# Performance work log

Measured on AMD Instinct MI355X. Metric: run time of the kernel, lower is better.

## Reference

```python
import jax, jax.numpy as jnp
import numpy as np

B, N, DIM, H, DH = 2, 2048, 512, 8, 64
INNER = H * DH  # == DIM, required by the q.view trick in the original module
STEP = 4


def setup_inputs() -> dict:
    key = jax.random.key(0)
    k1, k2, k3 = jax.random.split(key, 3)
    x = jax.random.normal(k1, (B, N, DIM), jnp.float32)
    # to_qkv: Linear(dim, 4*inner_dim, bias=False); stored as [in, out] for x @ W
    W_qkv = jax.random.normal(k2, (DIM, 4 * INNER), jnp.float32) * 0.02
    # to_out: Linear(2*inner_dim, dim) with bias
    W_out = jax.random.normal(k3, (2 * INNER, DIM), jnp.float32) * 0.02
    b_out = jnp.zeros((DIM,), jnp.float32)
    return {"x": x, "W_qkv": W_qkv, "W_out": W_out, "b_out": b_out}


def reference(x, W_qkv, W_out, b_out):
    b, n, _ = x.shape
    h, dh = H, DH
    scale = dh ** -0.5

    qkvt = x @ W_qkv                       # [b, n, 4*inner]
    q, k, v, t = jnp.split(qkvt, 4, axis=-1)
    to_heads = lambda z: z.reshape(b, n, h, dh).transpose(0, 2, 1, 3)  # [b,h,n,dh]
    q, k, v, t = map(to_heads, (q, k, v, t))

    # pad q by repeating its last row yushu times (note: yushu=4 when n%4==0)
    yushu = STEP - n % STEP
    q = jnp.concatenate([q, jnp.repeat(q[:, :, -1:, :], yushu, axis=2)], axis=2)
    q0 = q.reshape(b, h, STEP, (n + yushu) // STEP, dh)[:, :, 0]  # [b,h,(n+yushu)/4,dh]
    q = jnp.tile(q0, (1, 1, STEP, 1))[:, :, :n]                   # [b,h,n,dh]

    dots = jnp.einsum('bhnd,bhmd->bhnm', q, k) * scale
    attn1 = jax.nn.softmax(dots, axis=-1)

    # fixed distance-decay attention: exp(-|i-j|/e), column-normalized
    pos = jnp.arange(1, n + 1, dtype=x.dtype)
    tg = jnp.abs(pos[None, :] - pos[:, None])                     # [n, n]
    attn2 = jnp.exp(-tg / jnp.exp(jnp.asarray(1.0, x.dtype)))
    # torch: attn2 / attn2.sum(-1) broadcasts [n] over last axis (divides column j by row-sum j)
    attn2 = attn2 / attn2.sum(-1)

    out1 = jnp.einsum('bhnm,bhmd->bhnd', attn1, v)
    out2 = jnp.einsum('nm,bhmd->bhnd', attn2, t)  # attn2 shared across b,h; no repeat needed
    out = jnp.concatenate([out1, out2], axis=-1)   # [b,h,n,2*dh]
    out = out.transpose(0, 2, 1, 3).reshape(b, n, 2 * h * dh)  # b n (h d)
    return out @ W_out + b_out  # dropout=0.0 -> identity
```

## Files before the change

### kernel.cpp

```cpp
#include <hip/hip_runtime.h>

#define NSEQ 2048
#define NB   2
#define NH   8

typedef unsigned short u16;
typedef __attribute__((ext_vector_type(8))) short s8v;
typedef __attribute__((ext_vector_type(4))) float f4v;

static __device__ __forceinline__ u16 f2bf(float f) {
  unsigned u = __float_as_uint(f);
  unsigned r = (u + 0x7fffu + ((u >> 16) & 1u)) >> 16;
  return (u16)r;
}
static __device__ __forceinline__ unsigned pk2(float a, float b) {
  return (unsigned)f2bf(a) | ((unsigned)f2bf(b) << 16);
}
static __device__ __forceinline__ float bf2f(u16 v) {
  return __uint_as_float(((unsigned)v) << 16);
}

typedef __attribute__((address_space(3))) unsigned int lds_u32;
typedef const __attribute__((address_space(1))) unsigned int glob_u32;
static __device__ __forceinline__ void load16(const void* g, void* l) {
  __builtin_amdgcn_global_load_lds((glob_u32*)g, (lds_u32*)l, 16, 0, 0);
}

__global__ __launch_bounds__(256)
void prep_kernel(const float* __restrict__ x, const float* __restrict__ Wqkv,
                 const float* __restrict__ Wout, u16* __restrict__ xb,
                 u16* __restrict__ WqkvT, u16* __restrict__ Wc) {
  __shared__ float tile[32][33];
  const int bid = blockIdx.x;
  if (bid < 1024) {
    long i = ((long)bid * 256 + threadIdx.x) * 8;
    float4 a = *(const float4*)&x[i];
    float4 b = *(const float4*)&x[i + 4];
    uint4 w;
    w.x = pk2(a.x, a.y); w.y = pk2(a.z, a.w);
    w.z = pk2(b.x, b.y); w.w = pk2(b.z, b.w);
    *(uint4*)&xb[i] = w;
    return;
  }
  const int tx = threadIdx.x & 31, ty = threadIdx.x >> 5;
  if (bid < 2048) {
    int b2 = bid - 1024;
    int c0 = (b2 & 63) * 32, r0 = (b2 >> 6) * 32;
#pragma unroll
    for (int s = 0; s < 32; s += 8)
      tile[ty + s][tx] = Wqkv[(long)(r0 + ty + s) * 2048 + c0 + tx];
    __syncthreads();
#pragma unroll
    for (int s = 0; s < 32; s += 8)
      WqkvT[(long)(c0 + ty + s) * 512 + r0 + tx] = f2bf(tile[tx][ty + s]);
    return;
  }
  {
    int b3 = bid - 2048;
    int part = b3 >= 256;
    if (part) b3 -= 256;
    int c0 = (b3 & 15) * 32, r0 = (b3 >> 4) * 32;
#pragma unroll
    for (int s = 0; s < 32; s += 8) {
      int k = r0 + ty + s;
      int srcrow = ((k >> 6) * 128) + part * 64 + (k & 63);
      tile[ty + s][tx] = Wout[(long)srcrow * 512 + c0 + tx];
    }
    __syncthreads();
    int koff = part ? 0 : 512;
#pragma unroll
    for (int s = 0; s < 32; s += 8) {
      long o = (long)(c0 + ty + s) * 1024 + koff + r0 + tx;
      Wc[o] = f2bf(tile[tx][ty + s]);
    }
  }
}

__global__ __launch_bounds__(256)
void gemm1_fused(const u16* __restrict__ xb, const u16* __restrict__ WqkvT,
                 u16* __restrict__ qkvtb, u16* __restrict__ qu,
                 u16* __restrict__ VtG) {
  const int bx = blockIdx.x, by = blockIdx.y;
  const bool isq = bx >= 12;
  if (isq && by >= 9) return;
  __shared__ alignas(16) u16 As[128 * 32];
  __shared__ alignas(16) u16 Bs[128 * 32];
  const int tid = threadIdx.x, lane = tid & 63, wave = tid >> 6;
  const int l15 = lane & 15, quad = lane >> 4;
  const int wr = wave >> 1, wc = wave & 1;
  const int Brow0 = isq ? (bx - 12) * 128 : 512 + bx * 128;

  f4v acc[4][4];
#pragma unroll
  for (int i = 0; i < 4; ++i)
#pragma unroll
    for (int j = 0; j < 4; ++j) acc[i][j] = (f4v){0.f, 0.f, 0.f, 0.f};

  for (int k0 = 0; k0 < 512; k0 += 32) {
    __syncthreads();
#pragma unroll
    for (int c = 0; c < 2; ++c) {
      int off = (c * 4 + wave) * 1024 + lane * 16;
      int r = off >> 6, cb = (off & 63) >> 1;
      int gar;
      if (!isq) {
        gar = by * 128 + r;
      } else {
        int rr = by * 128 + r;
        int b = rr >= 576;
        int s = rr - (b ? 576 : 0);
        if (s >= 513) s -= 513;
        gar = b * 2048 + s;
      }
      load16(&xb[(long)gar * 512 + k0 + cb], ((char*)As) + off);
      load16(&WqkvT[(long)(Brow0 + r) * 512 + k0 + cb], ((char*)Bs) + off);
    }
    __syncthreads();

    s8v bf[4];
#pragma unroll
    for (int j = 0; j < 4; ++j)
      bf[j] = *(const s8v*)&Bs[(wc * 64 + j * 16 + l15) * 32 + quad * 8];
#pragma unroll
    for (int i = 0; i < 4; ++i) {
      s8v af = *(const s8v*)&As[(wr * 64 + i * 16 + l15) * 32 + quad * 8];
#pragma unroll
      for (int j = 0; j < 4; ++j)
        acc[i][j] = __builtin_amdgcn_mfma_f32_16x16x32_bf16(af, bf[j], acc[i][j], 0, 0, 0);
    }
  }

  const bool isv = (!isq) && bx >= 4 && bx < 8;
#pragma unroll
  for (int i = 0; i < 4; ++i) {
    int row0 = by * 128 + wr * 64 + i * 16 + quad * 4;
    if (isv) {
      int b = row0 >> 11, n = row0 & 2047;
#pragma unroll
      for (int j = 0; j < 4; ++j) {
        int vcol = (bx - 4) * 128 + wc * 64 + j * 16 + l15;
        int h = vcol >> 6, d = vcol & 63;
        uint2 w;
        w.x = pk2(acc[i][j][0], acc[i][j][1]);
        w.y = pk2(acc[i][j][2], acc[i][j][3]);
        *(uint2*)&VtG[(((long)b * 8 + h) * 64 + d) * 2048 + n] = w;
      }
    } else {
#pragma unroll
      for (int rr = 0; rr < 4; ++rr) {
        int row = row0 + rr;
#pragma unroll
        for (int j = 0; j < 4; ++j) {
          int col = wc * 64 + j * 16 + l15;
          u16 v = f2bf(acc[i][j][rr]);
          if (!isq)
            qkvtb[(long)row * 2048 + 512 + bx * 128 + col] = v;
          else
            qu[(long)row * 512 + (bx - 12) * 128 + col] = v;
        }
      }
    }
  }
}

__global__ __launch_bounds__(256)
void gemm2_merged(const u16* __restrict__ O2, const u16* __restrict__ O1u,
                  const u16* __restrict__ Wc, const float* __restrict__ bias,
                  float* __restrict__ C) {
  __shared__ alignas(16) u16 As[128 * 32];
  __shared__ alignas(16) u16 Bs[64 * 32];
  const int tid = threadIdx.x, lane = tid & 63, wave = tid >> 6;
  const int l15 = lane & 15, quad = lane >> 4;
  const int wr = wave >> 1, wc = wave & 1;
  const long m0 = (long)blockIdx.y * 128, n0 = (long)blockIdx.x * 64;

  long baseO2[2], baseO1[2];
  int offA[2];
#pragma unroll
  for (int c = 0; c < 2; ++c) {
    int off = (c * 4 + wave) * 1024 + lane * 16;
    int r = off >> 6, cb = (off & 63) >> 1;
    offA[c] = off;
    long rowA = m0 + r;
    int b = (int)(rowA >> 11);
    int eff = (int)(rowA & 2047) % 513;
    baseO2[c] = rowA * 512 + cb;
    baseO1[c] = ((long)(b * 576 + eff)) * 512 + cb;
  }
  const int offB = wave * 1024 + lane * 16;
  const long baseB = (long)(n0 + (offB >> 6)) * 1024 + ((offB & 63) >> 1);

  f4v acc[4][2];
#pragma unroll
  for (int i = 0; i < 4; ++i)
#pragma unroll
    for (int j = 0; j < 2; ++j) acc[i][j] = (f4v){0.f, 0.f, 0.f, 0.f};

  for (int k0 = 0; k0 < 1024; k0 += 32) {
    __syncthreads();
#pragma unroll
    for (int c = 0; c < 2; ++c) {
      const u16* src = (k0 < 512) ? &O2[baseO2[c] + k0] : &O1u[baseO1[c] + k0 - 512];
      load16(src, ((char*)As) + offA[c]);
    }
    load16(&Wc[baseB + k0], ((char*)Bs) + offB);
    __syncthreads();

    s8v bf[2];
#pragma unroll
    for (int j = 0; j < 2; ++j)
      bf[j] = *(const s8v*)&Bs[(wc * 32 + j * 16 + l15) * 32 + quad * 8];
#pragma unroll
    for (int i = 0; i < 4; ++i) {
      s8v af = *(const s8v*)&As[(wr * 64 + i * 16 + l15) * 32 + quad * 8];
#pragma unroll
      for (int j = 0; j < 2; ++j)
        acc[i][j] = __builtin_amdgcn_mfma_f32_16x16x32_bf16(af, bf[j], acc[i][j], 0, 0, 0);
    }
  }

#pragma unroll
  for (int i = 0; i < 4; ++i)
#pragma unroll
    for (int rr = 0; rr < 4; ++rr) {
      long row = m0 + wr * 64 + i * 16 + quad * 4 + rr;
#pragma unroll
      for (int j = 0; j < 2; ++j) {
        long col = n0 + wc * 32 + j * 16 + l15;
        C[row * 512 + col] = acc[i][j][rr] + bias[col];
      }
    }
}

__global__ __launch_bounds__(256)
void attn_kernel(const u16* __restrict__ qkvt, const u16* __restrict__ qu,
                 const u16* __restrict__ VtG, float* __restrict__ Opart,
                 float* __restrict__ rspart) {
  __shared__ alignas(16) u16 Qs[64 * 64];
  __shared__ alignas(16) u16 Ks[64 * 64];
  __shared__ alignas(16) u16 Vt[64 * 64];
  __shared__ alignas(16) u16 Ps[4][16][72];

  const int tid  = threadIdx.x;
  const int lane = tid & 63, wave = tid >> 6;
  const int l15  = lane & 15, quad = lane >> 4;
  const int qtile = blockIdx.x;
  const int bh = blockIdx.y;
  const int split = blockIdx.z;
  const int b = bh >> 3, h = bh & 7;
  const long rowbase = (long)b * NSEQ;
  const long vtbase = ((long)b * 8 + h) * 64 * 2048;

  int srow[2], scs[2];
#pragma unroll
  for (int p = 0; p < 2; ++p) {
    int idx = p * 256 + tid;
    srow[p] = idx >> 3;
    scs[p] = (idx & 7) ^ (srow[p] & 7);
  }

#pragma unroll
  for (int p = 0; p < 2; ++p) {
    int v = qtile * 64 + srow[p];
    int eff = v >= 513 ? v - 513 : v;
    load16(&qu[((long)(b * 576 + eff)) * 512 + h * 64 + scs[p] * 8],
           (char*)Qs + (p * 256 + wave * 64) * 16);
  }
  __syncthreads();

  s8v qf[2];
  {
    const int mrow = wave * 16 + l15;
    const int c0 = quad ^ (mrow & 7);
    qf[0] = *(const s8v*)&Qs[mrow * 64 + c0 * 8];
    qf[1] = *(const s8v*)&Qs[mrow * 64 + (c0 ^ 4) * 8];
  }

  f4v oacc[4];
#pragma unroll
  for (int i = 0; i < 4; ++i) oacc[i] = (f4v){0.f, 0.f, 0.f, 0.f};
  float rs[4] = {0.f, 0.f, 0.f, 0.f};

  for (int kt = 0; kt < 8; ++kt) {
    __syncthreads();
    const int kb = split * 512 + kt * 64;
#pragma unroll
    for (int p = 0; p < 2; ++p) {
      load16(&qkvt[(rowbase + kb + srow[p]) * 2048 + 512 + h * 64 + scs[p] * 8],
             (char*)Ks + (p * 256 + wave * 64) * 16);
      load16(&VtG[vtbase + (long)srow[p] * 2048 + kb + scs[p] * 8],
             (char*)Vt + (p * 256 + wave * 64) * 16);
    }
    __syncthreads();

#pragma unroll
    for (int nt = 0; nt < 4; ++nt) {
      f4v s = {0.f, 0.f, 0.f, 0.f};
      const int kr = nt * 16 + l15;
      const int kc0 = quad ^ (kr & 7);
      s8v kf0 = *(const s8v*)&Ks[kr * 64 + kc0 * 8];
      s8v kf1 = *(const s8v*)&Ks[kr * 64 + (kc0 ^ 4) * 8];
      s = __builtin_amdgcn_mfma_f32_16x16x32_bf16(qf[0], kf0, s, 0, 0, 0);
      s = __builtin_amdgcn_mfma_f32_16x16x32_bf16(qf[1], kf1, s, 0, 0, 0);
#pragma unroll
      for (int rr = 0; rr < 4; ++rr) {
        float p = __expf(s[rr] * 0.125f);
        rs[rr] += p;
        Ps[wave][quad * 4 + rr][nt * 16 + l15] = f2bf(p);
      }
    }
    asm volatile("" ::: "memory");

    s8v pf0 = *(const s8v*)&Ps[wave][l15][quad * 8];
    s8v pf1 = *(const s8v*)&Ps[wave][l15][32 + quad * 8];
#pragma unroll
    for (int nt = 0; nt < 4; ++nt) {
      const int vr = nt * 16 + l15;
      const int vc0 = quad ^ (vr & 7);
      s8v vf0 = *(const s8v*)&Vt[vr * 64 + vc0 * 8];
      s8v vf1 = *(const s8v*)&Vt[vr * 64 + (vc0 ^ 4) * 8];
      oacc[nt] = __builtin_amdgcn_mfma_f32_16x16x32_bf16(pf0, vf0, oacc[nt], 0, 0, 0);
      oacc[nt] = __builtin_amdgcn_mfma_f32_16x16x32_bf16(pf1, vf1, oacc[nt], 0, 0, 0);
    }
  }

  const long sb = ((long)split * 16 + bh) * 576;
#pragma unroll
  for (int rr = 0; rr < 4; ++rr) {
    float t = rs[rr];
    t += __shfl_xor(t, 1);
    t += __shfl_xor(t, 2);
    t += __shfl_xor(t, 4);
    t += __shfl_xor(t, 8);
    int row = qtile * 64 + wave * 16 + quad * 4 + rr;
    if (l15 == 0) rspart[sb + row] = t;
#pragma unroll
    for (int nt = 0; nt < 4; ++nt)
      Opart[(sb + row) * 64 + nt * 16 + l15] = oacc[nt][rr];
  }
}

__global__ __launch_bounds__(256)
void post_kernel(const u16* __restrict__ qkvt, const float* __restrict__ Opart,
                 const float* __restrict__ rspart, u16* __restrict__ O1u,
                 u16* __restrict__ O2) {
  __shared__ u16 Ts[256 * 64];
  __shared__ float Is[256];
  const int tid = threadIdx.x;
  const int bid = blockIdx.x;
  if (bid >= 512) {
    int idx = (bid - 512) * 256 + tid;
    int d4 = idx & 15, rowbh = idx >> 4;
    int bh = rowbh / 576, row = rowbh - bh * 576;
    int b = bh >> 3, h = bh & 7;
    float4 o = {0.f, 0.f, 0.f, 0.f};
    float rsum = 0.f;
#pragma unroll
    for (int s = 0; s < 4; ++s) {
      long base = ((long)s * 16 + bh) * 576 + row;
      float4 v = *(const float4*)&Opart[base * 64 + d4 * 4];
      o.x += v.x; o.y += v.y; o.z += v.z; o.w += v.w;
      rsum += rspart[base];
    }
    float inv = 1.0f / rsum;
    uint2 w = {pk2(o.x * inv, o.y * inv), pk2(o.z * inv, o.w * inv)};
    *(uint2*)&O1u[((long)(b * 576 + row)) * 512 + h * 64 + d4 * 4] = w;
    return;
  }
  const int rg = bid & 31;
  const int bh = bid >> 5;
  const int b = bh >> 3, h = bh & 7;
  const int g0 = rg * 64 - 96;
#pragma unroll
  for (int c = 0; c < 8; ++c) {
    int chunk = c * 256 + tid;
    int row = chunk >> 3, cc = chunk & 7;
    int gr = g0 + row;
    uint4 w = {0u, 0u, 0u, 0u};
    if (gr >= 0 && gr < NSEQ)
      w = *(const uint4*)&qkvt[((long)(b * NSEQ + gr)) * 2048 + 1536 + h * 64 + cc * 8];
    *(uint4*)&Ts[row * 64 + cc * 8] = w;
  }
  {
    const float ie = 0.36787944117144233f;
    const float rr = 0.69220062755534635f;
    const float inv1mr = 1.0f / (1.0f - rr);
    int gr = g0 + tid;
    float val = 0.f;
    if (gr >= 0 && gr < NSEQ) {
      float rj = __expf(-ie * (float)gr);
      float rn = __expf(-ie * (float)(NSEQ - 1 - gr));
      float s = 1.0f + (rr - rr * rj) * inv1mr + (rr - rr * rn) * inv1mr;
      val = 1.0f / s;
    }
    Is[tid] = val;
  }
  __syncthreads();

  const int d = tid & 63, sub = tid >> 6;
  const float r = 0.69220062755534635f;
  const int lo = 96 + sub * 16;
  float F = 0.f;
  float Fv[16];
#pragma unroll 8
  for (int j = lo - 96; j < lo; ++j)
    F = F * r + Is[j] * bf2f(Ts[j * 64 + d]);
#pragma unroll
  for (int k = 0; k < 16; ++k) {
    int j = lo + k;
    F = F * r + Is[j] * bf2f(Ts[j * 64 + d]);
    Fv[k] = F;
  }
  float G = 0.f;
#pragma unroll 8
  for (int j = lo + 15 + 96; j > lo + 15; --j)
    G = G * r + Is[j] * bf2f(Ts[j * 64 + d]);
#pragma unroll
  for (int k = 15; k >= 0; --k) {
    int j = lo + k;
    float u = Is[j] * bf2f(Ts[j * 64 + d]);
    G = G * r + u;
    O2[((long)(b * NSEQ + g0 + j)) * 512 + h * 64 + d] = f2bf(Fv[k] + G - u);
  }
}

extern "C" void kernel_launch(void* const* d_in, const int* in_sizes, int n_in,
                              void* d_out, int out_size, void* d_ws, size_t ws_size,
                              hipStream_t stream) {
  (void)in_sizes; (void)n_in; (void)out_size; (void)ws_size;
  const float* x    = (const float*)d_in[0];
  const float* Wqkv = (const float*)d_in[1];
  const float* Wout = (const float*)d_in[2];
  const float* bout = (const float*)d_in[3];
  float* out = (float*)d_out;

  u16*   qkvtb = (u16*)d_ws;
  u16*   qu    = qkvtb + (size_t)4096 * 2048;
  u16*   VtG   = qu    + (size_t)1152 * 512;
  u16*   O2    = VtG   + (size_t)2 * 8 * 64 * 2048;
  u16*   O1u   = O2    + (size_t)4096 * 512;
  u16*   xb    = O1u   + (size_t)1152 * 512;
  u16*   WqkvT = xb    + (size_t)4096 * 512;
  u16*   Wc    = WqkvT + (size_t)2048 * 512;
  float* Opart = (float*)(Wc + (size_t)512 * 1024);
  float* rsp   = Opart + (size_t)4 * 16 * 576 * 64;

  prep_kernel<<<dim3(2560), 256, 0, stream>>>(x, Wqkv, Wout, xb, WqkvT, Wc);
  gemm1_fused<<<dim3(16, 32), 256, 0, stream>>>(xb, WqkvT, qkvtb, qu, VtG);
  attn_kernel<<<dim3(9, 16, 4), 256, 0, stream>>>(qkvtb, qu, VtG, Opart, rsp);
  post_kernel<<<dim3(1088), 256, 0, stream>>>(qkvtb, Opart, rsp, O1u, O2);
  gemm2_merged<<<dim3(8, 32), 256, 0, stream>>>(O2, O1u, Wc, bout, out);
}
```

Baseline: 132.9 us.

## Double GEMM K-tile with swizzled LDS, co-schedule out2 with attention, bf16 partials

Both GEMM kernels now stage 64-wide K tiles in XOR-swizzled shared memory, which halves the number of barrier pairs and avoids bank conflicts. The distance-decay (out2) work moves out of the post kernel into the attention launch as extra blocks that share a union of shared memory, so it runs alongside the softmax attention blocks. The remaining combine step becomes its own small kernel. Attention partial outputs are stored as bf16 instead of fp32, which cuts partial-buffer traffic at some precision cost. The larger shared footprint may lower occupancy.

```diff
diff --git a/kernel.cpp b/kernel.cpp
--- a/kernel.cpp
+++ b/kernel.cpp
@@ -83,50 +83,65 @@
   const int bx = blockIdx.x, by = blockIdx.y;
   const bool isq = bx >= 12;
   if (isq && by >= 9) return;
-  __shared__ alignas(16) u16 As[128 * 32];
-  __shared__ alignas(16) u16 Bs[128 * 32];
+  __shared__ alignas(16) u16 As[128 * 64];
+  __shared__ alignas(16) u16 Bs[128 * 64];
   const int tid = threadIdx.x, lane = tid & 63, wave = tid >> 6;
   const int l15 = lane & 15, quad = lane >> 4;
   const int wr = wave >> 1, wc = wave & 1;
   const int Brow0 = isq ? (bx - 12) * 128 : 512 + bx * 128;
 
+  int offv[4];
+  long baseA[4], baseB[4];
+#pragma unroll
+  for (int c = 0; c < 4; ++c) {
+    int off = (c * 4 + wave) * 1024 + lane * 16;
+    int r = off >> 7;
+    int cp = (off & 127) >> 4;
+    int cb = ((cp ^ (r & 7)) << 3);
+    offv[c] = off;
+    int gar;
+    if (!isq) {
+      gar = by * 128 + r;
+    } else {
+      int rr = by * 128 + r;
+      int b = rr >= 576;
+      int s = rr - (b ? 576 : 0);
+      if (s >= 513) s -= 513;
+      gar = b * 2048 + s;
+    }
+    baseA[c] = (long)gar * 512 + cb;
+    baseB[c] = (long)(Brow0 + r) * 512 + cb;
+  }
+
   f4v acc[4][4];
 #pragma unroll
   for (int i = 0; i < 4; ++i)
 #pragma unroll
     for (int j = 0; j < 4; ++j) acc[i][j] = (f4v){0.f, 0.f, 0.f, 0.f};
 
-  for (int k0 = 0; k0 < 512; k0 += 32) {
-    __syncthreads();
-#pragma unroll
-    for (int c = 0; c < 2; ++c) {
-      int off = (c * 4 + wave) * 1024 + lane * 16;
-      int r = off >> 6, cb = (off & 63) >> 1;
-      int gar;
-      if (!isq) {
-        gar = by * 128 + r;
-      } else {
-        int rr = by * 128 + r;
-        int b = rr >= 576;
-        int s = rr - (b ? 576 : 0);
-        if (s >= 513) s -= 513;
-        gar = b * 2048 + s;
-      }
-      load16(&xb[(long)gar * 512 + k0 + cb], ((char*)As) + off);
-      load16(&WqkvT[(long)(Brow0 + r) * 512 + k0 + cb], ((char*)Bs) + off);
-    }
-    __syncthreads();
-
-    s8v bf[4];
-#pragma unroll
-    for (int j = 0; j < 4; ++j)
-      bf[j] = *(const s8v*)&Bs[(wc * 64 + j * 16 + l15) * 32 + quad * 8];
-#pragma unroll
-    for (int i = 0; i < 4; ++i) {
-      s8v af = *(const s8v*)&As[(wr * 64 + i * 16 + l15) * 32 + quad * 8];
+  for (int k0 = 0; k0 < 512; k0 += 64) {
+    __syncthreads();
+#pragma unroll
+    for (int c = 0; c < 4; ++c) {
+      load16(&xb[baseA[c] + k0], ((char*)As) + offv[c]);
+      load16(&WqkvT[baseB[c] + k0], ((char*)Bs) + offv[c]);
+    }
+    __syncthreads();
+
+#pragma unroll
+    for (int ksub = 0; ksub < 2; ++ksub) {
+      const int cc = (((ksub << 2) | quad) ^ (l15 & 7)) << 3;
+      s8v bf[4];
 #pragma unroll
       for (int j = 0; j < 4; ++j)
-        acc[i][j] = __builtin_amdgcn_mfma_f32_16x16x32_bf16(af, bf[j], acc[i][j], 0, 0, 0);
+        bf[j] = *(const s8v*)&Bs[(wc * 64 + j * 16 + l15) * 64 + cc];
+#pragma unroll
+      for (int i = 0; i < 4; ++i) {
+        s8v af = *(const s8v*)&As[(wr * 64 + i * 16 + l15) * 64 + cc];
+#pragma unroll
+        for (int j = 0; j < 4; ++j)
+          acc[i][j] = __builtin_amdgcn_mfma_f32_16x16x32_bf16(af, bf[j], acc[i][j], 0, 0, 0);
+      }
     }
   }
 
@@ -167,19 +182,20 @@
 void gemm2_merged(const u16* __restrict__ O2, const u16* __restrict__ O1u,
                   const u16* __restrict__ Wc, const float* __restrict__ bias,
                   float* __restrict__ C) {
-  __shared__ alignas(16) u16 As[128 * 32];
-  __shared__ alignas(16) u16 Bs[64 * 32];
+  __shared__ alignas(16) u16 As[128 * 64];
+  __shared__ alignas(16) u16 Bs[64 * 64];
   const int tid = threadIdx.x, lane = tid & 63, wave = tid >> 6;
   const int l15 = lane & 15, quad = lane >> 4;
   const int wr = wave >> 1, wc = wave & 1;
   const long m0 = (long)blockIdx.y * 128, n0 = (long)blockIdx.x * 64;
 
-  long baseO2[2], baseO1[2];
-  int offA[2];
-#pragma unroll
-  for (int c = 0; c < 2; ++c) {
+  int offA[4];
+  long baseO2[4], baseO1[4];
+#pragma unroll
+  for (int c = 0; c < 4; ++c) {
     int off = (c * 4 + wave) * 1024 + lane * 16;
-    int r = off >> 6, cb = (off & 63) >> 1;
+    int r = off >> 7, cp = (off & 127) >> 4;
+    int cb = ((cp ^ (r & 7)) << 3);
     offA[c] = off;
     long rowA = m0 + r;
     int b = (int)(rowA >> 11);
@@ -187,8 +203,16 @@
     baseO2[c] = rowA * 512 + cb;
     baseO1[c] = ((long)(b * 576 + eff)) * 512 + cb;
   }
-  const int offB = wave * 1024 + lane * 16;
-  const long baseB = (long)(n0 + (offB >> 6)) * 1024 + ((offB & 63) >> 1);
+  int offB[2];
+  long baseB[2];
+#pragma unroll
+  for (int c = 0; c < 2; ++c) {
+    int off = (c * 4 + wave) * 1024 + lane * 16;
+    int r = off >> 7, cp = (off & 127) >> 4;
+    int cb = ((cp ^ (r & 7)) << 3);
+    offB[c] = off;
+    baseB[c] = (long)(n0 + r) * 1024 + cb;
+  }
 
   f4v acc[4][2];
 #pragma unroll
@@ -196,26 +220,32 @@
 #pragma unroll
     for (int j = 0; j < 2; ++j) acc[i][j] = (f4v){0.f, 0.f, 0.f, 0.f};
 
-  for (int k0 = 0; k0 < 1024; k0 += 32) {
-    __syncthreads();
-#pragma unroll
-    for (int c = 0; c < 2; ++c) {
+  for (int k0 = 0; k0 < 1024; k0 += 64) {
+    __syncthreads();
+#pragma unroll
+    for (int c = 0; c < 4; ++c) {
       const u16* src = (k0 < 512) ? &O2[baseO2[c] + k0] : &O1u[baseO1[c] + k0 - 512];
       load16(src, ((char*)As) + offA[c]);
     }
-    load16(&Wc[baseB + k0], ((char*)Bs) + offB);
-    __syncthreads();
-
-    s8v bf[2];
-#pragma unroll
-    for (int j = 0; j < 2; ++j)
-      bf[j] = *(const s8v*)&Bs[(wc * 32 + j * 16 + l15) * 32 + quad * 8];
-#pragma unroll
-    for (int i = 0; i < 4; ++i) {
-      s8v af = *(const s8v*)&As[(wr * 64 + i * 16 + l15) * 32 + quad * 8];
+#pragma unroll
+    for (int c = 0; c < 2; ++c)
+      load16(&Wc[baseB[c] + k0], ((char*)Bs) + offB[c]);
+    __syncthreads();
+
+#pragma unroll
+    for (int ksub = 0; ksub < 2; ++ksub) {
+      const int cc = (((ksub << 2) | quad) ^ (l15 & 7)) << 3;
+      s8v bf[2];
 #pragma unroll
       for (int j = 0; j < 2; ++j)
-        acc[i][j] = __builtin_amdgcn_mfma_f32_16x16x32_bf16(af, bf[j], acc[i][j], 0, 0, 0);
+        bf[j] = *(const s8v*)&Bs[(wc * 32 + j * 16 + l15) * 64 + cc];
+#pragma unroll
+      for (int i = 0; i < 4; ++i) {
+        s8v af = *(const s8v*)&As[(wr * 64 + i * 16 + l15) * 64 + cc];
+#pragma unroll
+        for (int j = 0; j < 2; ++j)
+          acc[i][j] = __builtin_amdgcn_mfma_f32_16x16x32_bf16(af, bf[j], acc[i][j], 0, 0, 0);
+      }
     }
   }
 
@@ -232,21 +262,91 @@
     }
 }
 
+struct AttnSm {
+  alignas(16) u16 Qs[64 * 64];
+  alignas(16) u16 Ks[64 * 64];
+  alignas(16) u16 Vt[64 * 64];
+  alignas(16) u16 Ps[4][16][72];
+};
+struct Out2Sm {
+  alignas(16) u16 Ts[256 * 64];
+  float Is[256];
+};
+
 __global__ __launch_bounds__(256)
-void attn_kernel(const u16* __restrict__ qkvt, const u16* __restrict__ qu,
-                 const u16* __restrict__ VtG, float* __restrict__ Opart,
-                 float* __restrict__ rspart) {
-  __shared__ alignas(16) u16 Qs[64 * 64];
-  __shared__ alignas(16) u16 Ks[64 * 64];
-  __shared__ alignas(16) u16 Vt[64 * 64];
-  __shared__ alignas(16) u16 Ps[4][16][72];
-
-  const int tid  = threadIdx.x;
+void attn_out2(const u16* __restrict__ qkvt, const u16* __restrict__ qu,
+               const u16* __restrict__ VtG, u16* __restrict__ Opart,
+               float* __restrict__ rspart, u16* __restrict__ O2) {
+  __shared__ union { AttnSm a; Out2Sm o; } sm;
+  const int tid = threadIdx.x;
+  const int bid = blockIdx.x;
+
+  if (bid >= 576) {
+    const int bid2 = bid - 576;
+    const int rg = bid2 & 31;
+    const int bh = bid2 >> 5;
+    const int b = bh >> 3, h = bh & 7;
+    const int g0 = rg * 64 - 96;
+#pragma unroll
+    for (int c = 0; c < 8; ++c) {
+      int chunk = c * 256 + tid;
+      int row = chunk >> 3, cc = chunk & 7;
+      int gr = g0 + row;
+      uint4 w = {0u, 0u, 0u, 0u};
+      if (gr >= 0 && gr < NSEQ)
+        w = *(const uint4*)&qkvt[((long)(b * NSEQ + gr)) * 2048 + 1536 + h * 64 + cc * 8];
+      *(uint4*)&sm.o.Ts[row * 64 + cc * 8] = w;
+    }
+    {
+      const float ie = 0.36787944117144233f;
+      const float rr = 0.69220062755534635f;
+      const float inv1mr = 1.0f / (1.0f - rr);
+      int gr = g0 + tid;
+      float val = 0.f;
+      if (gr >= 0 && gr < NSEQ) {
+        float rj = __expf(-ie * (float)gr);
+        float rn = __expf(-ie * (float)(NSEQ - 1 - gr));
+        float s = 1.0f + (rr - rr * rj) * inv1mr + (rr - rr * rn) * inv1mr;
+        val = 1.0f / s;
+      }
+      sm.o.Is[tid] = val;
+    }
+    __syncthreads();
+
+    const int d = tid & 63, sub = tid >> 6;
+    const float r = 0.69220062755534635f;
+    const int lo = 96 + sub * 16;
+    float F = 0.f;
+    float Fv[16];
+#pragma unroll 8
+    for (int j = lo - 96; j < lo; ++j)
+      F = F * r + sm.o.Is[j] * bf2f(sm.o.Ts[j * 64 + d]);
+#pragma unroll
+    for (int k = 0; k < 16; ++k) {
+      int j = lo + k;
+      F = F * r + sm.o.Is[j] * bf2f(sm.o.Ts[j * 64 + d]);
+      Fv[k] = F;
+    }
+    float G = 0.f;
+#pragma unroll 8
+    for (int j = lo + 15 + 96; j > lo + 15; --j)
+      G = G * r + sm.o.Is[j] * bf2f(sm.o.Ts[j * 64 + d]);
+#pragma unroll
+    for (int k = 15; k >= 0; --k) {
+      int j = lo + k;
+      float u = sm.o.Is[j] * bf2f(sm.o.Ts[j * 64 + d]);
+      G = G * r + u;
+      O2[((long)(b * NSEQ + g0 + j)) * 512 + h * 64 + d] = f2bf(Fv[k] + G - u);
+    }
+    return;
+  }
+
   const int lane = tid & 63, wave = tid >> 6;
   const int l15  = lane & 15, quad = lane >> 4;
-  const int qtile = blockIdx.x;
-  const int bh = blockIdx.y;
-  const int split = blockIdx.z;
+  const int qtile = bid % 9;
+  const int t9 = bid / 9;
+  const int bh = t9 & 15;
+  const int split = t9 >> 4;
   const int b = bh >> 3, h = bh & 7;
   const long rowbase = (long)b * NSEQ;
   const long vtbase = ((long)b * 8 + h) * 64 * 2048;
@@ -264,7 +364,7 @@
     int v = qtile * 64 + srow[p];
     int eff = v >= 513 ? v - 513 : v;
     load16(&qu[((long)(b * 576 + eff)) * 512 + h * 64 + scs[p] * 8],
-           (char*)Qs + (p * 256 + wave * 64) * 16);
+           (char*)sm.a.Qs + (p * 256 + wave * 64) * 16);
   }
   __syncthreads();
 
@@ -272,8 +372,8 @@
   {
     const int mrow = wave * 16 + l15;
     const int c0 = quad ^ (mrow & 7);
-    qf[0] = *(const s8v*)&Qs[mrow * 64 + c0 * 8];
-    qf[1] = *(const s8v*)&Qs[mrow * 64 + (c0 ^ 4) * 8];
+    qf[0] = *(const s8v*)&sm.a.Qs[mrow * 64 + c0 * 8];
+    qf[1] = *(const s8v*)&sm.a.Qs[mrow * 64 + (c0 ^ 4) * 8];
   }
 
   f4v oacc[4];
@@ -287,9 +387,9 @@
 #pragma unroll
     for (int p = 0; p < 2; ++p) {
       load16(&qkvt[(rowbase + kb + srow[p]) * 2048 + 512 + h * 64 + scs[p] * 8],
-             (char*)Ks + (p * 256 + wave * 64) * 16);
+             (char*)sm.a.Ks + (p * 256 + wave * 64) * 16);
       load16(&VtG[vtbase + (long)srow[p] * 2048 + kb + scs[p] * 8],
-             (char*)Vt + (p * 256 + wave * 64) * 16);
+             (char*)sm.a.Vt + (p * 256 + wave * 64) * 16);
     }
     __syncthreads();
 
@@ -298,27 +398,27 @@
       f4v s = {0.f, 0.f, 0.f, 0.f};
       const int kr = nt * 16 + l15;
       const int kc0 = quad ^ (kr & 7);
-      s8v kf0 = *(const s8v*)&Ks[kr * 64 + kc0 * 8];
-      s8v kf1 = *(const s8v*)&Ks[kr * 64 + (kc0 ^ 4) * 8];
+      s8v kf0 = *(const s8v*)&sm.a.Ks[kr * 64 + kc0 * 8];
+      s8v kf1 = *(const s8v*)&sm.a.Ks[kr * 64 + (kc0 ^ 4) * 8];
       s = __builtin_amdgcn_mfma_f32_16x16x32_bf16(qf[0], kf0, s, 0, 0, 0);
       s = __builtin_amdgcn_mfma_f32_16x16x32_bf16(qf[1], kf1, s, 0, 0, 0);
 #pragma unroll
       for (int rr = 0; rr < 4; ++rr) {
         float p = __expf(s[rr] * 0.125f);
         rs[rr] += p;
-        Ps[wave][quad * 4 + rr][nt * 16 + l15] = f2bf(p);
+        sm.a.Ps[wave][quad * 4 + rr][nt * 16 + l15] = f2bf(p);
       }
     }
     asm volatile("" ::: "memory");
 
-    s8v pf0 = *(const s8v*)&Ps[wave][l15][quad * 8];
-    s8v pf1 = *(const s8v*)&Ps[wave][l15][32 + quad * 8];
+    s8v pf0 = *(const s8v*)&sm.a.Ps[wave][l15][quad * 8];
+    s8v pf1 = *(const s8v*)&sm.a.Ps[wave][l15][32 + quad * 8];
 #pragma unroll
     for (int nt = 0; nt < 4; ++nt) {
       const int vr = nt * 16 + l15;
       const int vc0 = quad ^ (vr & 7);
-      s8v vf0 = *(const s8v*)&Vt[vr * 64 + vc0 * 8];
-      s8v vf1 = *(const s8v*)&Vt[vr * 64 + (vc0 ^ 4) * 8];
+      s8v vf0 = *(const s8v*)&sm.a.Vt[vr * 64 + vc0 * 8];
+      s8v vf1 = *(const s8v*)&sm.a.Vt[vr * 64 + (vc0 ^ 4) * 8];
       oacc[nt] = __builtin_amdgcn_mfma_f32_16x16x32_bf16(pf0, vf0, oacc[nt], 0, 0, 0);
       oacc[nt] = __builtin_amdgcn_mfma_f32_16x16x32_bf16(pf1, vf1, oacc[nt], 0, 0, 0);
     }
@@ -336,92 +436,33 @@
     if (l15 == 0) rspart[sb + row] = t;
 #pragma unroll
     for (int nt = 0; nt < 4; ++nt)
-      Opart[(sb + row) * 64 + nt * 16 + l15] = oacc[nt][rr];
+      Opart[(sb + row) * 64 + nt * 16 + l15] = f2bf(oacc[nt][rr]);
   }
 }
 
 __global__ __launch_bounds__(256)
-void post_kernel(const u16* __restrict__ qkvt, const float* __restrict__ Opart,
-                 const float* __restrict__ rspart, u16* __restrict__ O1u,
-                 u16* __restrict__ O2) {
-  __shared__ u16 Ts[256 * 64];
-  __shared__ float Is[256];
-  const int tid = threadIdx.x;
-  const int bid = blockIdx.x;
-  if (bid >= 512) {
-    int idx = (bid - 512) * 256 + tid;
-    int d4 = idx & 15, rowbh = idx >> 4;
-    int bh = rowbh / 576, row = rowbh - bh * 576;
-    int b = bh >> 3, h = bh & 7;
-    float4 o = {0.f, 0.f, 0.f, 0.f};
-    float rsum = 0.f;
-#pragma unroll
-    for (int s = 0; s < 4; ++s) {
-      long base = ((long)s * 16 + bh) * 576 + row;
-      float4 v = *(const float4*)&Opart[base * 64 + d4 * 4];
-      o.x += v.x; o.y += v.y; o.z += v.z; o.w += v.w;
-      rsum += rspart[base];
-    }
-    float inv = 1.0f / rsum;
-    uint2 w = {pk2(o.x * inv, o.y * inv), pk2(o.z * inv, o.w * inv)};
-    *(uint2*)&O1u[((long)(b * 576 + row)) * 512 + h * 64 + d4 * 4] = w;
-    return;
-  }
-  const int rg = bid & 31;
-  const int bh = bid >> 5;
-  const int b = bh >> 3, h = bh & 7;
-  const int g0 = rg * 64 - 96;
-#pragma unroll
-  for (int c = 0; c < 8; ++c) {
-    int chunk = c * 256 + tid;
-    int row = chunk >> 3, cc = chunk & 7;
-    int gr = g0 + row;
-    uint4 w = {0u, 0u, 0u, 0u};
-    if (gr >= 0 && gr < NSEQ)
-      w = *(const uint4*)&qkvt[((long)(b * NSEQ + gr)) * 2048 + 1536 + h * 64 + cc * 8];
-    *(uint4*)&Ts[row * 64 + cc * 8] = w;
-  }
-  {
-    const float ie = 0.36787944117144233f;
-    const float rr = 0.69220062755534635f;
-    const float inv1mr = 1.0f / (1.0f - rr);
-    int gr = g0 + tid;
-    float val = 0.f;
-    if (gr >= 0 && gr < NSEQ) {
-      float rj = __expf(-ie * (float)gr);
-      float rn = __expf(-ie * (float)(NSEQ - 1 - gr));
-      float s = 1.0f + (rr - rr * rj) * inv1mr + (rr - rr * rn) * inv1mr;
-      val = 1.0f / s;
-    }
-    Is[tid] = val;
-  }
-  __syncthreads();
-
-  const int d = tid & 63, sub = tid >> 6;
-  const float r = 0.69220062755534635f;
-  const int lo = 96 + sub * 16;
-  float F = 0.f;
-  float Fv[16];
-#pragma unroll 8
-  for (int j = lo - 96; j < lo; ++j)
-    F = F * r + Is[j] * bf2f(Ts[j * 64 + d]);
-#pragma unroll
-  for (int k = 0; k < 16; ++k) {
-    int j = lo + k;
-    F = F * r + Is[j] * bf2f(Ts[j * 64 + d]);
-    Fv[k] = F;
-  }
-  float G = 0.f;
-#pragma unroll 8
-  for (int j = lo + 15 + 96; j > lo + 15; --j)
-    G = G * r + Is[j] * bf2f(Ts[j * 64 + d]);
-#pragma unroll
-  for (int k = 15; k >= 0; --k) {
-    int j = lo + k;
-    float u = Is[j] * bf2f(Ts[j * 64 + d]);
-    G = G * r + u;
-    O2[((long)(b * NSEQ + g0 + j)) * 512 + h * 64 + d] = f2bf(Fv[k] + G - u);
-  }
+void attn_combine(const u16* __restrict__ Opart, const float* __restrict__ rspart,
+                  u16* __restrict__ O1u) {
+  int idx = blockIdx.x * 256 + threadIdx.x;
+  int d4 = idx & 15, rowbh = idx >> 4;
+  int bh = rowbh / 576, row = rowbh - bh * 576;
+  int b = bh >> 3, h = bh & 7;
+  float o[4] = {0.f, 0.f, 0.f, 0.f};
+  float rsum = 0.f;
+#pragma unroll
+  for (int s = 0; s < 4; ++s) {
+    long base = ((long)s * 16 + bh) * 576 + row;
+    const u16* p = &Opart[base * 64 + d4 * 4];
+    uint2 v = *(const uint2*)p;
+    o[0] += bf2f((u16)(v.x & 0xffff));
+    o[1] += bf2f((u16)(v.x >> 16));
+    o[2] += bf2f((u16)(v.y & 0xffff));
+    o[3] += bf2f((u16)(v.y >> 16));
+    rsum += rspart[base];
+  }
+  float inv = 1.0f / rsum;
+  uint2 w = {pk2(o[0] * inv, o[1] * inv), pk2(o[2] * inv, o[3] * inv)};
+  *(uint2*)&O1u[((long)(b * 576 + row)) * 512 + h * 64 + d4 * 4] = w;
 }
 
 extern "C" void kernel_launch(void* const* d_in, const int* in_sizes, int n_in,
@@ -442,12 +483,12 @@
   u16*   xb    = O1u   + (size_t)1152 * 512;
   u16*   WqkvT = xb    + (size_t)4096 * 512;
   u16*   Wc    = WqkvT + (size_t)2048 * 512;
-  float* Opart = (float*)(Wc + (size_t)512 * 1024);
-  float* rsp   = Opart + (size_t)4 * 16 * 576 * 64;
+  u16*   Opart = Wc    + (size_t)512 * 1024;
+  float* rsp   = (float*)(Opart + (size_t)4 * 16 * 576 * 64);
 
   prep_kernel<<<dim3(2560), 256, 0, stream>>>(x, Wqkv, Wout, xb, WqkvT, Wc);
   gemm1_fused<<<dim3(16, 32), 256, 0, stream>>>(xb, WqkvT, qkvtb, qu, VtG);
-  attn_kernel<<<dim3(9, 16, 4), 256, 0, stream>>>(qkvtb, qu, VtG, Opart, rsp);
-  post_kernel<<<dim3(1088), 256, 0, stream>>>(qkvtb, Opart, rsp, O1u, O2);
+  attn_out2<<<dim3(1088), 256, 0, stream>>>(qkvtb, qu, VtG, Opart, rsp, O2);
+  attn_combine<<<dim3(576), 256, 0, stream>>>(Opart, rsp, O1u);
   gemm2_merged<<<dim3(8, 32), 256, 0, stream>>>(O2, O1u, Wc, bout, out);
 }
```

Result: faster. 125.9 us (-5.3%).
